# Performance work log

Measured on AMD Instinct MI355X. Metric: run time of the kernel, lower is better.

The kernel has to match this reference:

```python
import jax, jax.numpy as jnp
import numpy as np

N, D, F, K = 50000, 256, 256, 10


def setup_inputs() -> dict:
    key = jax.random.key(0)
    k1, k2, k3, k4, k5, k6 = jax.random.split(key, 6)
    # neighbor indices in [-1, N); -1 marks padding (masked out in forward)
    return {
        "Z1": jax.random.normal(k1, (N, D), dtype=jnp.float32),
        "Z2": jax.random.normal(k2, (N, D), dtype=jnp.float32),
        "Wr": jax.random.normal(k3, (D, F), dtype=jnp.float32),
        "Wnr": jax.random.normal(k4, (D, F), dtype=jnp.float32),
        "n1": jax.random.randint(k5, (N, K), -1, N, dtype=jnp.int64),
        "n2": jax.random.randint(k6, (N, K), -1, N, dtype=jnp.int64),
    }


def _protein(Z, nb, Wr, Wnr):
    residues_signal = Z @ Wr                      # [N, F]
    neighbors_base_signal = Z @ Wnr               # [N, F]
    mask = (nb > -1)                              # [N, K]
    # index -1 wraps to last row (as in torch), then is zeroed by the mask
    feats = neighbors_base_signal[nb] * mask[..., None].astype(Z.dtype)  # [N, K, F]
    norm = jnp.maximum(mask.sum(axis=1), 1).astype(Z.dtype)[:, None]     # [N, 1]
    neighbors_signal = feats.sum(axis=1) / norm
    return jax.nn.relu(residues_signal + neighbors_signal)


def reference(Z1, Z2, Wr, Wnr, n1, n2):
    out1 = _protein(Z1, n1, Wr, Wnr)
    out2 = _protein(Z2, n2, Wr, Wnr)
    return jnp.stack([out1, out2])  # [2, N, F]
```

## Files before the change

kernel.cpp:

```cpp
#include <hip/hip_runtime.h>
#include <hip/hip_bf16.h>
#include <hip/hip_fp8.h>

#define NNODE 50000
#define MTOT  100000
#define NF    256
#define KNB   10

typedef unsigned short u16;
typedef float f32x4 __attribute__((ext_vector_type(4)));
typedef float f32x2 __attribute__((ext_vector_type(2)));
typedef short bf16x8 __attribute__((ext_vector_type(8)));

__device__ __forceinline__ u16 f2bf(float f) {
    unsigned u = __builtin_bit_cast(unsigned, f);
    unsigned r = (u + 0x7fffu + ((u >> 16) & 1u)) >> 16;
    return (u16)r;
}
__device__ __forceinline__ unsigned char f2f8(float f) {
    return (unsigned char)__hip_fp8_e4m3(f).__x;
}
__device__ __forceinline__ float f8tof(unsigned char b) {
    __hip_fp8_e4m3 h;
    h.__x = (__hip_fp8_storage_t)b;
    return (float)h;
}
template <int WORD>
__device__ __forceinline__ f32x2 cvt2_fp8(unsigned v) {
#if __has_builtin(__builtin_amdgcn_cvt_pk_f32_fp8)
    auto c = __builtin_amdgcn_cvt_pk_f32_fp8((int)v, WORD);
    f32x2 r; r.x = c[0]; r.y = c[1];
    return r;
#else
    unsigned s = WORD ? (v >> 16) : v;
    f32x2 r;
    r.x = f8tof((unsigned char)(s & 0xff));
    r.y = f8tof((unsigned char)((s >> 8) & 0xff));
    return r;
#endif
}
__device__ __forceinline__ void gload_lds16(const void* g, void* l) {
    __builtin_amdgcn_global_load_lds(
        (const __attribute__((address_space(1))) unsigned int*)g,
        (__attribute__((address_space(3))) unsigned int*)l, 16, 0, 0);
}

__global__ __launch_bounds__(256) void cast_all(const float* __restrict__ Z1,
                                                const float* __restrict__ Z2,
                                                const float* __restrict__ Wr,
                                                const float* __restrict__ Wnr,
                                                u16* __restrict__ Zleft,
                                                unsigned char* __restrict__ Z8,
                                                u16* __restrict__ WT) {
    int b = blockIdx.x;
    if (b < 12500) {
        unsigned id = b * 256 + threadIdx.x;
        int m = id >> 5;
        int d = (id & 31) << 3;
        const float* src = (m < NNODE) ? (Z1 + (size_t)m * 256 + d)
                                       : (Z2 + (size_t)(m - NNODE) * 256 + d);
        float4 a = *(const float4*)src;
        float4 bb = *(const float4*)(src + 4);
        uint4 o;
        o.x = (unsigned)f2bf(a.x) | ((unsigned)f2bf(a.y) << 16);
        o.y = (unsigned)f2bf(a.z) | ((unsigned)f2bf(a.w) << 16);
        o.z = (unsigned)f2bf(bb.x) | ((unsigned)f2bf(bb.y) << 16);
        o.w = (unsigned)f2bf(bb.z) | ((unsigned)f2bf(bb.w) << 16);
        *(uint4*)(Zleft + (size_t)m * 256 + d) = o;
        uint2 o8;
        o8.x = (unsigned)f2f8(a.x) | ((unsigned)f2f8(a.y) << 8) |
               ((unsigned)f2f8(a.z) << 16) | ((unsigned)f2f8(a.w) << 24);
        o8.y = (unsigned)f2f8(bb.x) | ((unsigned)f2f8(bb.y) << 8) |
               ((unsigned)f2f8(bb.z) << 16) | ((unsigned)f2f8(bb.w) << 24);
        *(uint2*)(Z8 + (size_t)m * 256 + d) = o8;
    } else {
        int id = (b - 12500) * 256 + threadIdx.x;
        int n = id >> 9;
        int k = id & 511;
        float v = (k < 256) ? Wr[(size_t)k * 256 + n] : Wnr[(size_t)(k - 256) * 256 + n];
        WT[(size_t)n * 512 + k] = f2bf(v);
    }
}

__device__ __forceinline__ void stage_tileA(const u16* __restrict__ A, u16* dst,
                                            int m0, int kt, int t) {
    #pragma unroll
    for (int rp = 0; rp < 2; ++rp) {
        int c = rp * 512 + t;
        int row = c >> 3, gd = c & 7;
        int gs = gd ^ (row & 7);
        int grow = m0 + row;
        if (grow >= MTOT) grow = MTOT - 1;
        gload_lds16(A + (size_t)grow * 256 + kt + gs * 8, dst + c * 8);
    }
}
__device__ __forceinline__ void stage_tileB(const u16* __restrict__ BT, u16* dst,
                                            int kt, int t) {
    #pragma unroll
    for (int rp = 0; rp < 4; ++rp) {
        int c = rp * 512 + t;
        int col = c >> 3, gd = c & 7;
        int gs = gd ^ (col & 7);
        gload_lds16(BT + (size_t)col * 512 + kt + gs * 8, dst + c * 8);
    }
}

template <int GRPX>
__device__ __forceinline__ void gather_issue(const unsigned char* __restrict__ Z8,
                                             const int (&vidx)[3], int m0, int w,
                                             int vo, uchar4 (&buf)[40]) {
    constexpr int GRP = (GRPX > 3) ? 3 : GRPX;
    #pragma unroll
    for (int rr = 0; rr < 4; ++rr) {
        int g = m0 + (w << 4) + GRP * 4 + rr;
        if (g >= MTOT) g = MTOT - 1;
        g = __builtin_amdgcn_readfirstlane(g);
        const unsigned char* rb = Z8 + (size_t)(g >= NNODE) * ((size_t)NNODE * 256);
        #pragma unroll
        for (int k = 0; k < KNB; ++k) {
            int f = (GRP * 4 + rr) * 10 + k;
            int ix = __builtin_amdgcn_readlane(vidx[f >> 6], f & 63);
            int safe = (ix > -1) ? ix : 0;
            buf[rr * 10 + k] = *(const uchar4*)(rb + (size_t)safe * 256 + vo);
        }
    }
}

template <int GRPX>
__device__ __forceinline__ void consume_avg(const int (&vidx)[3], int w, int lane,
                                            const uchar4 (&buf)[40], u16* sZ) {
    constexpr int GRP = (GRPX > 3) ? 3 : GRPX;
    #pragma unroll
    for (int rr = 0; rr < 4; ++rr) {
        f32x2 a01 = {0.f, 0.f}, a23 = {0.f, 0.f};
        int cnt = 0;
        #pragma unroll
        for (int k = 0; k < KNB; ++k) {
            int f = (GRP * 4 + rr) * 10 + k;
            int ix = __builtin_amdgcn_readlane(vidx[f >> 6], f & 63);
            int valid = (ix > -1);
            cnt += valid;
            unsigned raw = __builtin_bit_cast(unsigned, buf[rr * 10 + k]);
            raw = valid ? raw : 0u;
            a01 += cvt2_fp8<0>(raw);
            a23 += cvt2_fp8<1>(raw);
        }
        float sc = 1.0f / (float)(cnt > 0 ? cnt : 1);
        int r = (w << 4) + GRP * 4 + rr;
        int gp = (lane >> 1) ^ (r & 7);
        ushort4 o;
        o.x = f2bf(a01.x * sc); o.y = f2bf(a01.y * sc);
        o.z = f2bf(a23.x * sc); o.w = f2bf(a23.y * sc);
        *(ushort4*)&sZ[r * 256 + gp * 8 + (lane & 1) * 4] = o;
    }
}

__device__ __forceinline__ void mfma_left(const u16* sAc, const u16* sBc, int lane,
                                          int wr, int wc, f32x4 (&acc)[4][4]) {
    const int l7 = lane & 7, l15 = lane & 15;
    #pragma unroll
    for (int kk = 0; kk < 64; kk += 32) {
        int kq = kk + ((lane >> 4) << 3);
        int gx = (kq >> 3) ^ l7;
        bf16x8 af[4], bfr[4];
        #pragma unroll
        for (int i = 0; i < 4; ++i)
            af[i] = *(const bf16x8*)&sAc[(wr * 64 + i * 16 + l15) * 64 + gx * 8];
        #pragma unroll
        for (int j = 0; j < 4; ++j)
            bfr[j] = *(const bf16x8*)&sBc[(wc * 64 + j * 16 + l15) * 64 + gx * 8];
        #pragma unroll
        for (int i = 0; i < 4; ++i)
            #pragma unroll
            for (int j = 0; j < 4; ++j)
                acc[i][j] = __builtin_amdgcn_mfma_f32_16x16x32_bf16(af[i], bfr[j], acc[i][j], 0, 0, 0);
    }
}
__device__ __forceinline__ void mfma_right(const u16* sZc, const u16* sBc, int kt0, int lane,
                                           int wr, int wc, f32x4 (&acc)[4][4]) {
    const int l7 = lane & 7, l15 = lane & 15;
    #pragma unroll
    for (int kk = 0; kk < 64; kk += 32) {
        int kq = kk + ((lane >> 4) << 3);
        int gx = (kq >> 3) ^ l7;
        int gzx = ((kt0 + kq) >> 3) ^ l7;
        bf16x8 af[4], bfr[4];
        #pragma unroll
        for (int i = 0; i < 4; ++i)
            af[i] = *(const bf16x8*)&sZc[(wr * 64 + i * 16 + l15) * 256 + gzx * 8];
        #pragma unroll
        for (int j = 0; j < 4; ++j)
            bfr[j] = *(const bf16x8*)&sBc[(wc * 64 + j * 16 + l15) * 64 + gx * 8];
        #pragma unroll
        for (int i = 0; i < 4; ++i)
            #pragma unroll
            for (int j = 0; j < 4; ++j)
                acc[i][j] = __builtin_amdgcn_mfma_f32_16x16x32_bf16(af[i], bfr[j], acc[i][j], 0, 0, 0);
    }
}

__global__ __launch_bounds__(512, 2) void gemm_fused(const u16* __restrict__ A,
                                                     const unsigned char* __restrict__ Z8,
                                                     const u16* __restrict__ BT,
                                                     const int* __restrict__ n1,
                                                     const int* __restrict__ n2,
                                                     float* __restrict__ C) {
    __shared__ u16 sA[2][128 * 64];
    __shared__ u16 sB[2][256 * 64];
    __shared__ u16 sZ[128 * 256];
    const int m0 = blockIdx.x * 128;
    const int t = threadIdx.x;
    const int lane = t & 63;
    const int w = t >> 6;
    const int wr = w >> 2, wc = w & 3;
    const int vo = lane * 4;

    f32x4 acc[4][4] = {};
    uchar4 gbuf[2][40];

    int vidx[3];
    #pragma unroll
    for (int j = 0; j < 3; ++j) {
        int f = lane + j * 64;
        if (f > 159) f = 159;
        int rl = f / 10;
        int kk2 = f - rl * 10;
        int g = m0 + (w << 4) + rl;
        if (g >= MTOT) g = MTOT - 1;
        int p = (g >= NNODE);
        vidx[j] = *((p ? n2 : n1) + (size_t)(g - p * NNODE) * KNB + kk2);
    }
    stage_tileA(A, &sA[0][0], m0, 0, t);
    stage_tileB(BT, &sB[0][0], 0, t);
    gather_issue<0>(Z8, vidx, m0, w, vo, gbuf[0]);

#define LEFT_STEP(S)                                                        \
    do {                                                                    \
        if ((S) < 3) {                                                      \
            gather_issue<(S) + 1>(Z8, vidx, m0, w, vo, gbuf[((S) + 1) & 1]);\
            stage_tileA(A, &sA[((S) + 1) & 1][0], m0, ((S) + 1) * 64, t);   \
            stage_tileB(BT, &sB[((S) + 1) & 1][0], ((S) + 1) * 64, t);      \
            asm volatile("s_waitcnt vmcnt(46)" ::: "memory");               \
        } else {                                                            \
            stage_tileB(BT, &sB[((S) + 1) & 1][0], 256, t);                 \
            asm volatile("s_waitcnt vmcnt(4)" ::: "memory");                \
        }                                                                   \
        __builtin_amdgcn_s_barrier();                                       \
        __builtin_amdgcn_s_setprio(1);                                      \
        mfma_left(&sA[(S) & 1][0], &sB[(S) & 1][0], lane, wr, wc, acc);     \
        __builtin_amdgcn_s_setprio(0);                                      \
        consume_avg<(S)>(vidx, w, lane, gbuf[(S) & 1], &sZ[0]);             \
        asm volatile("s_waitcnt lgkmcnt(0)" ::: "memory");                  \
        __builtin_amdgcn_s_barrier();                                       \
    } while (0)

    LEFT_STEP(0);
    LEFT_STEP(1);
    LEFT_STEP(2);
    LEFT_STEP(3);
#undef LEFT_STEP

#define RIGHT_STEP(S)                                                       \
    do {                                                                    \
        if ((S) < 7) {                                                      \
            stage_tileB(BT, &sB[((S) + 1) & 1][0], ((S) + 1) * 64, t);      \
            asm volatile("s_waitcnt vmcnt(4)" ::: "memory");                \
        } else {                                                            \
            asm volatile("s_waitcnt vmcnt(0)" ::: "memory");                \
        }                                                                   \
        __builtin_amdgcn_s_barrier();                                       \
        __builtin_amdgcn_s_setprio(1);                                      \
        mfma_right(&sZ[0], &sB[(S) & 1][0], ((S) - 4) * 64, lane, wr, wc, acc); \
        __builtin_amdgcn_s_setprio(0);                                      \
        if ((S) < 7) __builtin_amdgcn_s_barrier();                          \
    } while (0)

    RIGHT_STEP(4);
    RIGHT_STEP(5);
    RIGHT_STEP(6);
    RIGHT_STEP(7);
#undef RIGHT_STEP

    const int l15 = lane & 15;
    #pragma unroll
    for (int i = 0; i < 4; ++i) {
        int rbase = m0 + wr * 64 + i * 16 + ((lane >> 4) << 2);
        #pragma unroll
        for (int j = 0; j < 4; ++j) {
            int col = wc * 64 + j * 16 + l15;
            #pragma unroll
            for (int q = 0; q < 4; ++q) {
                int row = rbase + q;
                if (row < MTOT) C[(size_t)row * NF + col] = fmaxf(acc[i][j][q], 0.f);
            }
        }
    }
}

extern "C" void kernel_launch(void* const* d_in, const int* in_sizes, int n_in,
                              void* d_out, int out_size, void* d_ws, size_t ws_size,
                              hipStream_t stream) {
    const float* Z1  = (const float*)d_in[0];
    const float* Z2  = (const float*)d_in[1];
    const float* Wr  = (const float*)d_in[2];
    const float* Wnr = (const float*)d_in[3];
    const int*   n1  = (const int*)d_in[4];
    const int*   n2  = (const int*)d_in[5];
    float* out = (float*)d_out;

    u16* WT    = (u16*)d_ws;
    u16* Zleft = WT + 256 * 512;
    unsigned char* Z8 = (unsigned char*)(Zleft + (size_t)MTOT * 256);

    cast_all<<<13012, 256, 0, stream>>>(Z1, Z2, Wr, Wnr, Zleft, Z8, WT);
    gemm_fused<<<782, 512, 0, stream>>>(Zleft, Z8, WT, n1, n2, out);
}
```

Baseline: 131.4 us.

## Widen neighbor gather to 16-byte loads with per-lane row indices

Restructures the fused neighbor gather so each group of 16 lanes owns one row and loads 16-byte fp8 chunks per neighbor, instead of each wave loading 4 bytes per lane for four rows. Neighbor indices now go into per-lane registers through int2 loads, which replaces the readlane broadcasts. The averaged result is packed with v_cvt_pk_bf16_f32 into 16-byte LDS stores. Global loads in flight per step drop from 40 to 10 per thread, so the vmcnt wait thresholds and the lgkmcnt waits change to match, at the cost of more index registers.

```diff
diff --git a/kernel.cpp b/kernel.cpp
--- a/kernel.cpp
+++ b/kernel.cpp
@@ -38,6 +38,11 @@
     r.y = f8tof((unsigned char)((s >> 8) & 0xff));
     return r;
 #endif
+}
+__device__ __forceinline__ unsigned pack_bf16(float lo, float hi) {
+    unsigned r;
+    asm("v_cvt_pk_bf16_f32 %0, %1, %2" : "=v"(r) : "v"(lo), "v"(hi));
+    return r;
 }
 __device__ __forceinline__ void gload_lds16(const void* g, void* l) {
     __builtin_amdgcn_global_load_lds(
@@ -105,54 +110,49 @@
     }
 }
 
-template <int GRPX>
-__device__ __forceinline__ void gather_issue(const unsigned char* __restrict__ Z8,
-                                             const int (&vidx)[3], int m0, int w,
-                                             int vo, uchar4 (&buf)[40]) {
-    constexpr int GRP = (GRPX > 3) ? 3 : GRPX;
-    #pragma unroll
-    for (int rr = 0; rr < 4; ++rr) {
-        int g = m0 + (w << 4) + GRP * 4 + rr;
-        if (g >= MTOT) g = MTOT - 1;
-        g = __builtin_amdgcn_readfirstlane(g);
-        const unsigned char* rb = Z8 + (size_t)(g >= NNODE) * ((size_t)NNODE * 256);
-        #pragma unroll
-        for (int k = 0; k < KNB; ++k) {
-            int f = (GRP * 4 + rr) * 10 + k;
-            int ix = __builtin_amdgcn_readlane(vidx[f >> 6], f & 63);
-            int safe = (ix > -1) ? ix : 0;
-            buf[rr * 10 + k] = *(const uchar4*)(rb + (size_t)safe * 256 + vo);
-        }
-    }
-}
-
-template <int GRPX>
-__device__ __forceinline__ void consume_avg(const int (&vidx)[3], int w, int lane,
-                                            const uchar4 (&buf)[40], u16* sZ) {
-    constexpr int GRP = (GRPX > 3) ? 3 : GRPX;
-    #pragma unroll
-    for (int rr = 0; rr < 4; ++rr) {
-        f32x2 a01 = {0.f, 0.f}, a23 = {0.f, 0.f};
-        int cnt = 0;
-        #pragma unroll
-        for (int k = 0; k < KNB; ++k) {
-            int f = (GRP * 4 + rr) * 10 + k;
-            int ix = __builtin_amdgcn_readlane(vidx[f >> 6], f & 63);
-            int valid = (ix > -1);
-            cnt += valid;
-            unsigned raw = __builtin_bit_cast(unsigned, buf[rr * 10 + k]);
-            raw = valid ? raw : 0u;
-            a01 += cvt2_fp8<0>(raw);
-            a23 += cvt2_fp8<1>(raw);
-        }
-        float sc = 1.0f / (float)(cnt > 0 ? cnt : 1);
-        int r = (w << 4) + GRP * 4 + rr;
-        int gp = (lane >> 1) ^ (r & 7);
-        ushort4 o;
-        o.x = f2bf(a01.x * sc); o.y = f2bf(a01.y * sc);
-        o.z = f2bf(a23.x * sc); o.w = f2bf(a23.y * sc);
-        *(ushort4*)&sZ[r * 256 + gp * 8 + (lane & 1) * 4] = o;
-    }
+template <int S>
+__device__ __forceinline__ void gather_issue2(const unsigned char* __restrict__ Z8,
+                                              const int (&idxv)[4][KNB],
+                                              const unsigned (&rowoff)[4],
+                                              uint4 (&gb)[KNB]) {
+    #pragma unroll
+    for (int k = 0; k < KNB; ++k) {
+        int ix = idxv[S][k];
+        unsigned off = rowoff[S] + (unsigned)((ix > -1) ? ix : 0) * 256u;
+        gb[k] = *(const uint4*)(Z8 + (size_t)off);
+    }
+}
+
+template <int S>
+__device__ __forceinline__ void consume2(const int (&idxv)[4][KNB], int w, int lane,
+                                         const uint4 (&gb)[KNB], u16* sZ) {
+    f32x2 ac[8];
+    #pragma unroll
+    for (int j = 0; j < 8; ++j) ac[j] = f32x2{0.f, 0.f};
+    int cnt = 0;
+    #pragma unroll
+    for (int k = 0; k < KNB; ++k) {
+        int valid = (idxv[S][k] > -1);
+        cnt += valid;
+        float mm = (float)valid;
+        f32x2 m2 = {mm, mm};
+        uint4 v = gb[k];
+        ac[0] += m2 * cvt2_fp8<0>(v.x); ac[1] += m2 * cvt2_fp8<1>(v.x);
+        ac[2] += m2 * cvt2_fp8<0>(v.y); ac[3] += m2 * cvt2_fp8<1>(v.y);
+        ac[4] += m2 * cvt2_fp8<0>(v.z); ac[5] += m2 * cvt2_fp8<1>(v.z);
+        ac[6] += m2 * cvt2_fp8<0>(v.w); ac[7] += m2 * cvt2_fp8<1>(v.w);
+    }
+    float sc = 1.0f / (float)(cnt > 0 ? cnt : 1);
+    unsigned pw[8];
+    #pragma unroll
+    for (int j = 0; j < 8; ++j)
+        pw[j] = pack_bf16(ac[j].x * sc, ac[j].y * sc);
+    int r = (w << 4) + S * 4 + (lane >> 4);
+    int g0 = 2 * (lane & 15);
+    unsigned b0 = r * 512 + (((g0)     ^ (r & 7)) << 4);
+    unsigned b1 = r * 512 + (((g0 + 1) ^ (r & 7)) << 4);
+    *(uint4*)((char*)sZ + b0) = uint4{pw[0], pw[1], pw[2], pw[3]};
+    *(uint4*)((char*)sZ + b1) = uint4{pw[4], pw[5], pw[6], pw[7]};
 }
 
 __device__ __forceinline__ void mfma_left(const u16* sAc, const u16* sBc, int lane,
@@ -213,34 +213,39 @@
     const int lane = t & 63;
     const int w = t >> 6;
     const int wr = w >> 2, wc = w & 3;
-    const int vo = lane * 4;
 
     f32x4 acc[4][4] = {};
-    uchar4 gbuf[2][40];
-
-    int vidx[3];
-    #pragma unroll
-    for (int j = 0; j < 3; ++j) {
-        int f = lane + j * 64;
-        if (f > 159) f = 159;
-        int rl = f / 10;
-        int kk2 = f - rl * 10;
-        int g = m0 + (w << 4) + rl;
+    uint4 gbuf[2][KNB];
+
+    stage_tileA(A, &sA[0][0], m0, 0, t);
+    stage_tileB(BT, &sB[0][0], 0, t);
+
+    int idxv[4][KNB];
+    unsigned rowoff[4];
+    #pragma unroll
+    for (int s = 0; s < 4; ++s) {
+        int g = m0 + (w << 4) + s * 4 + (lane >> 4);
         if (g >= MTOT) g = MTOT - 1;
         int p = (g >= NNODE);
-        vidx[j] = *((p ? n2 : n1) + (size_t)(g - p * NNODE) * KNB + kk2);
-    }
-    stage_tileA(A, &sA[0][0], m0, 0, t);
-    stage_tileB(BT, &sB[0][0], 0, t);
-    gather_issue<0>(Z8, vidx, m0, w, vo, gbuf[0]);
+        const int* nb = (p ? n2 : n1) + (size_t)(g - p * NNODE) * KNB;
+        #pragma unroll
+        for (int q = 0; q < 5; ++q) {
+            int2 v = *(const int2*)(nb + 2 * q);
+            idxv[s][2 * q] = v.x;
+            idxv[s][2 * q + 1] = v.y;
+        }
+        rowoff[s] = (unsigned)p * (unsigned)(NNODE * 256) + (unsigned)((lane & 15) << 4);
+    }
+    gather_issue2<0>(Z8, idxv, rowoff, gbuf[0]);
 
 #define LEFT_STEP(S)                                                        \
     do {                                                                    \
         if ((S) < 3) {                                                      \
-            gather_issue<(S) + 1>(Z8, vidx, m0, w, vo, gbuf[((S) + 1) & 1]);\
             stage_tileA(A, &sA[((S) + 1) & 1][0], m0, ((S) + 1) * 64, t);   \
             stage_tileB(BT, &sB[((S) + 1) & 1][0], ((S) + 1) * 64, t);      \
-            asm volatile("s_waitcnt vmcnt(46)" ::: "memory");               \
+            gather_issue2<((S) < 3 ? (S) + 1 : 3)>(Z8, idxv, rowoff,        \
+                                                   gbuf[((S) + 1) & 1]);    \
+            asm volatile("s_waitcnt vmcnt(16)" ::: "memory");               \
         } else {                                                            \
             stage_tileB(BT, &sB[((S) + 1) & 1][0], 256, t);                 \
             asm volatile("s_waitcnt vmcnt(4)" ::: "memory");                \
@@ -249,8 +254,8 @@
         __builtin_amdgcn_s_setprio(1);                                      \
         mfma_left(&sA[(S) & 1][0], &sB[(S) & 1][0], lane, wr, wc, acc);     \
         __builtin_amdgcn_s_setprio(0);                                      \
-        consume_avg<(S)>(vidx, w, lane, gbuf[(S) & 1], &sZ[0]);             \
-        asm volatile("s_waitcnt lgkmcnt(0)" ::: "memory");                  \
+        consume2<(S)>(idxv, w, lane, gbuf[(S) & 1], &sZ[0]);                \
+        if ((S) == 3) asm volatile("s_waitcnt lgkmcnt(0)" ::: "memory");    \
         __builtin_amdgcn_s_barrier();                                       \
     } while (0)
 
```

Result: faster. 121.4 us (-7.6%).
